# Optimization experiments

Measured on AMD Instinct MI355X. Metric: run time of the kernel, lower is better.

Reference implementation:

```python
import jax, jax.numpy as jnp
import numpy as np

B, T, P = 32, 40, 12
E, H = 2048, 1024
A_DIM, ACT_DIM = 9, 8


def _xavier(key, shape):
    fan_out, fan_in = shape
    lim = float(np.sqrt(6.0 / (fan_in + fan_out)))
    return jax.random.uniform(key, shape, jnp.float32, -lim, lim)


def setup_inputs() -> dict:
    key = jax.random.key(0)
    ks = jax.random.split(key, 8)
    return {
        "feature": jax.random.normal(ks[0], (B, T, P, E), jnp.float32),
        "W_embed": _xavier(ks[1], (H, E)),
        "b_embed": jnp.zeros((H,), jnp.float32),
        "W_ih": _xavier(ks[2], (3 * H, H)),
        "W_hh": _xavier(ks[3], (3 * H, H)),
        "b_ih": jnp.zeros((3 * H,), jnp.float32),
        "b_hh": jnp.zeros((3 * H,), jnp.float32),
        "W_act": _xavier(ks[4], (A_DIM, H)),
        "b_act": jnp.zeros((A_DIM,), jnp.float32),
        "W_activ": _xavier(ks[5], (ACT_DIM, H)),
        "b_activ": jnp.zeros((ACT_DIM,), jnp.float32),
    }


def reference(feature, W_embed, b_embed, W_ih, W_hh, b_ih, b_hh,
              W_act, b_act, W_activ, b_activ):
    # embed: Linear + Tanh -> [B, T, P, H]
    x = jnp.tanh(jnp.einsum('btpe,he->btph', feature, W_embed) + b_embed)
    # precompute input-side GRU gates for all timesteps: [B, T, P, 3H]
    gx = jnp.einsum('btph,gh->btpg', x, W_ih) + b_ih

    def step(h, gx_t):  # h: [B, P, H], gx_t: [B, P, 3H]
        gh = jnp.einsum('bph,gh->bpg', h, W_hh) + b_hh
        xr, xz, xn = jnp.split(gx_t, 3, axis=-1)
        hr, hz, hn = jnp.split(gh, 3, axis=-1)
        r = jax.nn.sigmoid(xr + hr)
        z = jax.nn.sigmoid(xz + hz)
        n = jnp.tanh(xn + r * hn)
        h_new = (1.0 - z) * n + z * h
        return h_new, h_new

    h0 = jnp.zeros((feature.shape[0], feature.shape[2], W_hh.shape[1]), feature.dtype)
    _, hs = jax.lax.scan(step, h0, jnp.moveaxis(gx, 1, 0))  # hs: [T, B, P, H]
    hiddens = jnp.moveaxis(hs, 0, 1)  # [B, T, P, H]

    # per-person action logits; torch loop order is (batch, time, person)
    action_logits = (jnp.einsum('btph,ah->btpa', hiddens, W_act) + b_act
                     ).reshape(-1, W_act.shape[0])
    # MaxPool2d((P,1)) over person axis, then Linear
    pooled = hiddens.max(axis=2)  # [B, T, H]
    activity_logits = (jnp.einsum('bth,ah->bta', pooled, W_activ) + b_activ
                       ).reshape(-1, W_activ.shape[0])
    return action_logits, activity_logits
```

## Files before the change

### kernel.cpp

```cpp
#include <hip/hip_runtime.h>
#include <cstdint>

#define B_ 32
#define T_ 40
#define P_ 12
#define E_ 2048
#define H_ 1024
#define BP 384
#define M_ 15360

typedef _Float16 f16;
typedef _Float16 f16x8 __attribute__((ext_vector_type(8)));
typedef float f32x4 __attribute__((ext_vector_type(4)));

__device__ __forceinline__ void cp16(const void* g, void* l) {
    auto gp = (const __attribute__((address_space(1))) uint32_t*)(uintptr_t)g;
    auto lp = (__attribute__((address_space(3))) uint32_t*)(uint32_t)(uintptr_t)l;
    __builtin_amdgcn_global_load_lds(gp, lp, 16, 0, 0);
}

__device__ __forceinline__ void store_wt(f16* p, f16 v) {
    unsigned short u = __builtin_bit_cast(unsigned short, v);
    asm volatile("global_store_short %0, %1, off sc0 sc1" :: "v"(p), "v"(u) : "memory");
}

__device__ __forceinline__ float fast_tanh(float x) {
    return 1.f - 2.f / (__expf(2.f * x) + 1.f);
}
__device__ __forceinline__ float fast_sig(float x) {
    return 1.f / (1.f + __expf(-x));
}

#define CVT_N0 ((M_ * E_) / 8)
#define CVT_N1 (CVT_N0 + (H_ * E_) / 8)
#define CVT_N2 (CVT_N1 + (3 * H_ * H_) / 8)
#define CVT_N3 (CVT_N2 + (3 * H_ * H_) / 8)
__global__ __launch_bounds__(256) void cvt_all(const float* __restrict__ f,
                                               const float* __restrict__ we,
                                               const float* __restrict__ wih,
                                               const float* __restrict__ whh,
                                               f16* __restrict__ fo, f16* __restrict__ weo,
                                               f16* __restrict__ wiho, f16* __restrict__ whho) {
    int i = blockIdx.x * 256 + threadIdx.x;
    if (i >= CVT_N3) return;
    const float* src; f16* dst; int j;
    if (i < CVT_N0)      { src = f;   dst = fo;   j = i; }
    else if (i < CVT_N1) { src = we;  dst = weo;  j = i - CVT_N0; }
    else if (i < CVT_N2) { src = wih; dst = wiho; j = i - CVT_N1; }
    else                 { src = whh; dst = whho; j = i - CVT_N2; }
    const float4* in4 = (const float4*)src;
    float4 a = in4[2 * j], b = in4[2 * j + 1];
    f16x8 o = {(f16)a.x, (f16)a.y, (f16)a.z, (f16)a.w,
               (f16)b.x, (f16)b.y, (f16)b.z, (f16)b.w};
    ((f16x8*)dst)[j] = o;
}

template <int EPI>
__global__ __launch_bounds__(256) void gemm128(const f16* __restrict__ A,
                                               const f16* __restrict__ Bm,
                                               const float* __restrict__ bias,
                                               f16* __restrict__ out, int K, int N) {
    __shared__ f16 As[2][128 * 32];
    __shared__ f16 Bs[2][128 * 32];
    const int tid = threadIdx.x;
    const int w = tid >> 6, l = tid & 63;
    const int wm = w >> 1, wn = w & 1;
    const long arow0 = (long)blockIdx.x * 128;
    const long brow0 = (long)blockIdx.y * 128;
    const int srow = l >> 2, scol = (l & 3) * 8;

    const f16* aptr = A + (arow0 + srow) * (long)K + scol;
    const f16* bptr = Bm + (brow0 + srow) * (long)K + scol;

    f32x4 acc[4][4] = {};

#pragma unroll
    for (int s = 0; s < 2; ++s) {
        int slice = w + s * 4;
        cp16(aptr + (long)slice * 16 * K, (void*)(As[0] + slice * 512));
        cp16(bptr + (long)slice * 16 * K, (void*)(Bs[0] + slice * 512));
    }
    asm volatile("s_waitcnt vmcnt(0)" ::: "memory");
    __syncthreads();

    const int nt = K >> 5;
    for (int t = 0; t < nt; ++t) {
        const int cur = t & 1;
        if (t + 1 < nt) {
            const long k0 = (long)(t + 1) << 5;
#pragma unroll
            for (int s = 0; s < 2; ++s) {
                int slice = w + s * 4;
                cp16(aptr + (long)slice * 16 * K + k0, (void*)(As[cur ^ 1] + slice * 512));
                cp16(bptr + (long)slice * 16 * K + k0, (void*)(Bs[cur ^ 1] + slice * 512));
            }
        }
        f16x8 af[4], bf[4];
#pragma unroll
        for (int i = 0; i < 4; ++i)
            af[i] = *(const f16x8*)(As[cur] + (wm * 64 + i * 16 + (l & 15)) * 32 + (l >> 4) * 8);
#pragma unroll
        for (int j = 0; j < 4; ++j)
            bf[j] = *(const f16x8*)(Bs[cur] + (wn * 64 + j * 16 + (l & 15)) * 32 + (l >> 4) * 8);
#pragma unroll
        for (int i = 0; i < 4; ++i)
#pragma unroll
            for (int j = 0; j < 4; ++j)
                acc[i][j] = __builtin_amdgcn_mfma_f32_16x16x32_f16(af[i], bf[j], acc[i][j], 0, 0, 0);
        asm volatile("s_waitcnt vmcnt(0)" ::: "memory");
        __syncthreads();
    }

    const int colq = l & 15, rowq = (l >> 4) * 4;
#pragma unroll
    for (int i = 0; i < 4; ++i)
#pragma unroll
        for (int j = 0; j < 4; ++j)
#pragma unroll
            for (int r = 0; r < 4; ++r) {
                long m = arow0 + wm * 64 + i * 16 + rowq + r;
                int n = (int)brow0 + wn * 64 + j * 16 + colq;
                float v = acc[i][j][r] + bias[n];
                if (EPI == 0) {
                    out[m * N + n] = (f16)fast_tanh(v);
                } else {
                    int b = (int)(m / (T_ * P_));
                    int rem = (int)(m % (T_ * P_));
                    int t = rem / P_, p = rem % P_;
                    out[((long)t * BP + b * P_ + p) * N + n] = (f16)v;
                }
            }
}

__global__ __launch_bounds__(256) void gru_step(const f16* __restrict__ h16_in,
                                                f16* __restrict__ h16_out,
                                                float* __restrict__ h32,
                                                const f16* __restrict__ Whh,
                                                const float* __restrict__ b_hh,
                                                const f16* __restrict__ gx16,
                                                f16* __restrict__ hid16, int t) {
    __shared__ f16 As[32 * 32];
    __shared__ f16 Bs[3 * 64 * 32];
    const int tid = threadIdx.x;
    const int w = tid >> 6, l = tid & 63;
    const int m0 = blockIdx.x * 32, n0 = blockIdx.y * 64;
    const int srow = l >> 2, scol = (l & 3) * 8;

    f32x4 acc[3][2] = {};

    for (int k0 = 0; k0 < H_; k0 += 32) {
        __syncthreads();
        if (w < 2)
            cp16(h16_in + (m0 + w * 16 + srow) * H_ + k0 + scol, (void*)(As + w * 512));
#pragma unroll
        for (int q3 = 0; q3 < 3; ++q3) {
            int s = w + q3 * 4;
            int g = s >> 2, q = s & 3;
            cp16(Whh + (long)(g * H_ + n0 + q * 16 + srow) * H_ + k0 + scol,
                 (void*)(Bs + (g * 64 + q * 16) * 32));
        }
        __syncthreads();
        f16x8 af[2], bf[3];
#pragma unroll
        for (int i = 0; i < 2; ++i)
            af[i] = *(const f16x8*)(As + (i * 16 + (l & 15)) * 32 + (l >> 4) * 8);
#pragma unroll
        for (int g = 0; g < 3; ++g)
            bf[g] = *(const f16x8*)(Bs + (g * 64 + w * 16 + (l & 15)) * 32 + (l >> 4) * 8);
#pragma unroll
        for (int g = 0; g < 3; ++g)
#pragma unroll
            for (int i = 0; i < 2; ++i)
                acc[g][i] = __builtin_amdgcn_mfma_f32_16x16x32_f16(af[i], bf[g], acc[g][i], 0, 0, 0);
    }

    const int col = n0 + w * 16 + (l & 15);
    const long gxbase = (long)t * BP * 3072;
    const float bhr = b_hh[col], bhz = b_hh[H_ + col], bhn = b_hh[2 * H_ + col];
#pragma unroll
    for (int i = 0; i < 2; ++i)
#pragma unroll
        for (int r = 0; r < 4; ++r) {
            int m = m0 + i * 16 + (l >> 4) * 4 + r;
            float hr = acc[0][i][r] + bhr;
            float hz = acc[1][i][r] + bhz;
            float hn = acc[2][i][r] + bhn;
            long gxrow = gxbase + (long)m * 3072;
            float xr = (float)gx16[gxrow + col];
            float xz = (float)gx16[gxrow + H_ + col];
            float xn = (float)gx16[gxrow + 2 * H_ + col];
            float rr = fast_sig(xr + hr);
            float zz = fast_sig(xz + hz);
            float nn = fast_tanh(xn + rr * hn);
            float hp = h32[m * H_ + col];
            float hnew = (1.f - zz) * nn + zz * hp;
            h32[m * H_ + col] = hnew;
            h16_out[m * H_ + col] = (f16)hnew;
            int b = m / P_, p = m % P_;
            hid16[(((long)b * T_ + t) * P_ + p) * H_ + col] = (f16)hnew;
        }
}

#define GRU_GRID 256
#define GRU_THREADS 384
#define GRU_BLDS (48 * 1024 * 2)
#define GRU_ALDS (4 * 96 * 64 * 2)
#define GRU_LDS (GRU_BLDS + GRU_ALDS)
#define FLAG_STRIDE 16

__global__ __launch_bounds__(GRU_THREADS) void gru_persistent(
        const f16* __restrict__ Whh, const float* __restrict__ bhh,
        const f16* __restrict__ gx16, f16* __restrict__ hid16,
        int* __restrict__ flags) {
    extern __shared__ char lds[];
    char* const Asb = lds + GRU_BLDS;

    const int tid = threadIdx.x;
    const int w = tid >> 6, l = tid & 63;
    const int q = l >> 4;

    const int bid = blockIdx.x;
    const int x = bid & 7;
    const int rg = x >> 1;
    const int nb = (x & 1) * 32 + (bid >> 3);
    const int m0 = rg * 96;
    const int j0 = nb * 16;

    for (int c = tid; c < 6144; c += GRU_THREADS) {
        int r = c >> 7;
        int kc = (c & 127) * 8;
        int grow = (r >> 4) * H_ + j0 + (r & 15);
        f16x8 v = *(const f16x8*)(Whh + (long)grow * H_ + kc);
        *(f16x8*)(lds + r * 2048 + ((kc * 2) ^ ((r & 7) << 4))) = v;
    }

    const int arow_l = w * 16 + (l & 15);
    int a_off[2], b_off[3][2];
#pragma unroll
    for (int sub = 0; sub < 2; ++sub) {
        a_off[sub] = arow_l * 128 + (((sub * 32 + q * 8) * 2) ^ ((arow_l & 7) << 4));
#pragma unroll
        for (int g = 0; g < 3; ++g) {
            int br = g * 16 + (l & 15);
            b_off[g][sub] = br * 2048 + (((sub * 32 + q * 8) * 2) ^ ((br & 7) << 4));
        }
    }
    const int swz = ((l & 7) ^ (l >> 3)) << 3;
    const int mA1 = m0 + w * 16 + (l >> 3);
    const int mA2 = mA1 + 8;
    const long srcA1 = ((long)(mA1 / P_) * T_ * P_ + (mA1 % P_)) * H_ + swz;
    const long srcA2 = ((long)(mA2 / P_) * T_ * P_ + (mA2 % P_)) * H_ + swz;

    const int col = j0 + (l & 15);
    const float bhr = bhh[col], bhz = bhh[H_ + col], bhn = bhh[2 * H_ + col];
    const int mrow = m0 + w * 16 + q * 4;
    long dstrow[4];
#pragma unroll
    for (int r = 0; r < 4; ++r) {
        int m = mrow + r;
        dstrow[r] = ((long)(m / P_) * T_ * P_ + (m % P_)) * H_ + col;
    }

    float hval[4] = {0.f, 0.f, 0.f, 0.f};

    f16 pgr[4], pgz[4], pgn[4];
#pragma unroll
    for (int r = 0; r < 4; ++r) {
        const long row = (long)(mrow + r) * 3072 + col;
        pgr[r] = gx16[row];
        pgz[r] = gx16[row + H_];
        pgn[r] = gx16[row + 2 * H_];
    }
    __syncthreads();

    for (int t = 0; t < T_; ++t) {
        f32x4 acc0 = {}, acc1 = {}, acc2 = {};

        if (t > 0) {
            if (w == 0) {
                const int* fp = flags + (((rg << 6) + l) * FLAG_STRIDE);
                while (__hip_atomic_load(fp, __ATOMIC_RELAXED,
                                         __HIP_MEMORY_SCOPE_AGENT) < t) {
                    __builtin_amdgcn_s_sleep(2);
                }
                __builtin_amdgcn_fence(__ATOMIC_ACQUIRE, "agent");
            }
            __syncthreads();

            const f16* __restrict__ hsrc = hid16 + (long)(t - 1) * (P_ * H_);

#pragma unroll
            for (int s = 0; s < 3; ++s) {
                char* b = Asb + s * 12288 + w * 2048;
                cp16(hsrc + srcA1 + s * 64, b);
                cp16(hsrc + srcA2 + s * 64, b + 1024);
            }

#pragma unroll
            for (int kk = 0; kk < 16; ++kk) {
                asm volatile("s_waitcnt lgkmcnt(0)" ::: "memory");
                if (kk < 13) {
                    const int s = kk + 3;
                    char* b = Asb + (s & 3) * 12288 + w * 2048;
                    cp16(hsrc + srcA1 + s * 64, b);
                    cp16(hsrc + srcA2 + s * 64, b + 1024);
                    asm volatile("s_waitcnt vmcnt(6)" ::: "memory");
                } else if (kk == 13) {
                    asm volatile("s_waitcnt vmcnt(4)" ::: "memory");
                } else if (kk == 14) {
                    asm volatile("s_waitcnt vmcnt(2)" ::: "memory");
                } else {
                    asm volatile("s_waitcnt vmcnt(0)" ::: "memory");
                }
                __builtin_amdgcn_sched_barrier(0);
                const char* Ab = Asb + (kk & 3) * 12288;
#pragma unroll
                for (int sub = 0; sub < 2; ++sub) {
                    f16x8 af  = *(const f16x8*)(Ab + a_off[sub]);
                    f16x8 bf0 = *(const f16x8*)(lds + b_off[0][sub] + kk * 128);
                    f16x8 bf1 = *(const f16x8*)(lds + b_off[1][sub] + kk * 128);
                    f16x8 bf2 = *(const f16x8*)(lds + b_off[2][sub] + kk * 128);
                    acc0 = __builtin_amdgcn_mfma_f32_16x16x32_f16(af, bf0, acc0, 0, 0, 0);
                    acc1 = __builtin_amdgcn_mfma_f32_16x16x32_f16(af, bf1, acc1, 0, 0, 0);
                    acc2 = __builtin_amdgcn_mfma_f32_16x16x32_f16(af, bf2, acc2, 0, 0, 0);
                }
            }
        }

        const long toff = (long)t * (P_ * H_);
#pragma unroll
        for (int r = 0; r < 4; ++r) {
            float hr = acc0[r] + bhr;
            float hz = acc1[r] + bhz;
            float hn = acc2[r] + bhn;
            float rr = fast_sig((float)pgr[r] + hr);
            float zz = fast_sig((float)pgz[r] + hz);
            float nn = fast_tanh((float)pgn[r] + rr * hn);
            float hnew = (1.f - zz) * nn + zz * hval[r];
            hval[r] = hnew;
            store_wt(hid16 + toff + dstrow[r], (f16)hnew);
        }
        asm volatile("s_waitcnt vmcnt(0)" ::: "memory");
        __syncthreads();
        if (tid == 0) {
            __hip_atomic_store(flags + (((rg << 6) + nb) * FLAG_STRIDE), t + 1,
                               __ATOMIC_RELEASE, __HIP_MEMORY_SCOPE_AGENT);
        }

        if (t + 1 < T_) {
            const long gxb = (long)(t + 1) * BP * 3072 + col;
#pragma unroll
            for (int r = 0; r < 4; ++r) {
                const long row = gxb + (long)(mrow + r) * 3072;
                pgr[r] = gx16[row];
                pgz[r] = gx16[row + H_];
                pgn[r] = gx16[row + 2 * H_];
            }
        }
    }
}

__global__ __launch_bounds__(256) void logits_kernel(const f16* __restrict__ hid16,
                                                     const float* __restrict__ W_act,
                                                     const float* __restrict__ b_act,
                                                     const float* __restrict__ W_activ,
                                                     const float* __restrict__ b_activ,
                                                     float* __restrict__ out) {
    __shared__ f16 hs[P_ * H_];
    __shared__ float pooled[H_];
    const int bt = blockIdx.x;
    const int tid = threadIdx.x, w = tid >> 6, l = tid & 63;

    const f16x8* src = (const f16x8*)(hid16 + (long)bt * P_ * H_);
    f16x8* dst = (f16x8*)hs;
    for (int i = tid; i < P_ * H_ / 8; i += 256) dst[i] = src[i];
    __syncthreads();

    for (int i = tid; i < H_; i += 256) {
        float mx = (float)hs[i];
#pragma unroll
        for (int p = 1; p < P_; ++p) mx = fmaxf(mx, (float)hs[p * H_ + i]);
        pooled[i] = mx;
    }
    __syncthreads();

    for (int j = w; j < 108; j += 4) {
        int p = j / 9, a = j % 9;
        float s = 0.f;
#pragma unroll
        for (int it = 0; it < 16; ++it) {
            int idx = l + it * 64;
            s += (float)hs[p * H_ + idx] * W_act[a * H_ + idx];
        }
#pragma unroll
        for (int off = 32; off > 0; off >>= 1) s += __shfl_down(s, off);
        if (l == 0) out[((long)bt * P_ + p) * 9 + a] = s + b_act[a];
    }
    for (int j = w; j < 8; j += 4) {
        float s = 0.f;
#pragma unroll
        for (int it = 0; it < 16; ++it) {
            int idx = l + it * 64;
            s += pooled[idx] * W_activ[j * H_ + idx];
        }
#pragma unroll
        for (int off = 32; off > 0; off >>= 1) s += __shfl_down(s, off);
        if (l == 0) out[(long)M_ * 9 + (long)bt * 8 + j] = s + b_activ[j];
    }
}

extern "C" void kernel_launch(void* const* d_in, const int* in_sizes, int n_in,
                              void* d_out, int out_size, void* d_ws, size_t ws_size,
                              hipStream_t stream) {
    const float* feature = (const float*)d_in[0];
    const float* W_embed = (const float*)d_in[1];
    const float* b_embed = (const float*)d_in[2];
    const float* W_ih    = (const float*)d_in[3];
    const float* W_hh    = (const float*)d_in[4];
    const float* b_ih    = (const float*)d_in[5];
    const float* b_hh    = (const float*)d_in[6];
    const float* W_act   = (const float*)d_in[7];
    const float* b_act   = (const float*)d_in[8];
    const float* W_activ = (const float*)d_in[9];
    const float* b_activ = (const float*)d_in[10];
    float* out = (float*)d_out;

    char* ws = (char*)d_ws;
    size_t off = 0;
    auto alloc = [&](size_t bytes) {
        void* p = ws + off;
        off = (off + bytes + 255) & ~(size_t)255;
        return p;
    };
    f16*   feat16 = (f16*)alloc((size_t)M_ * E_ * 2);
    f16*   wE16   = (f16*)alloc((size_t)H_ * E_ * 2);
    f16*   wIH16  = (f16*)alloc((size_t)3 * H_ * H_ * 2);
    f16*   wHH16  = (f16*)alloc((size_t)3 * H_ * H_ * 2);
    f16*   x16    = (f16*)alloc((size_t)M_ * H_ * 2);
    f16*   gx16   = (f16*)alloc((size_t)M_ * 3 * H_ * 2);
    float* h32    = (float*)alloc((size_t)BP * H_ * 4);
    f16*   h16a   = (f16*)alloc((size_t)BP * H_ * 2);
    f16*   h16b   = (f16*)alloc((size_t)BP * H_ * 2);
    f16*   hid16  = (f16*)alloc((size_t)M_ * H_ * 2);
    int*   flags  = (int*)h32;
    (void)ws_size; (void)in_sizes; (void)n_in; (void)out_size;

    cvt_all<<<CVT_N3 / 256, 256, 0, stream>>>(feature, W_embed, W_ih, W_hh,
                                              feat16, wE16, wIH16, wHH16);

    gemm128<0><<<dim3(M_ / 128, H_ / 128), 256, 0, stream>>>(feat16, wE16, b_embed, x16, E_, H_);
    gemm128<1><<<dim3(M_ / 128, (3 * H_) / 128), 256, 0, stream>>>(x16, wIH16, b_ih, gx16, H_, 3 * H_);

    hipMemsetAsync(h32, 0, (size_t)BP * H_ * 4 + (size_t)BP * H_ * 2, stream);

    (void)hipFuncSetAttribute(reinterpret_cast<const void*>(gru_persistent),
                              hipFuncAttributeMaxDynamicSharedMemorySize, GRU_LDS);
    const f16* p_whh = wHH16; const float* p_bhh = b_hh; const f16* p_gx = gx16;
    f16* p_hid = hid16; int* p_flags = flags;
    void* kargs[] = {&p_whh, &p_bhh, &p_gx, &p_hid, &p_flags};
    hipError_t cerr = hipLaunchCooperativeKernel(
        reinterpret_cast<const void*>(gru_persistent),
        dim3(GRU_GRID), dim3(GRU_THREADS), kargs, GRU_LDS, stream);
    if (cerr != hipSuccess) {
        for (int t = 0; t < T_; ++t) {
            const f16* hin = (t & 1) ? h16b : h16a;
            f16* hout = (t & 1) ? h16a : h16b;
            gru_step<<<dim3(BP / 32, H_ / 64), 256, 0, stream>>>(hin, hout, h32, wHH16, b_hh,
                                                                 gx16, hid16, t);
        }
    }

    logits_kernel<<<B_ * T_, 256, 0, stream>>>(hid16, W_act, b_act, W_activ, b_activ, out);
}
```

Before: 929.5 us.

## Load GRU hidden-state operand straight into registers and relax store ordering

The recurrent GEMM in the persistent GRU kernel now loads the previous hidden state directly from global memory into registers: all 32 16-byte chunks are issued up front and then fed to the MFMAs. This replaces the 4-stage LDS ring filled with global_load_lds and its manual vmcnt/lgkmcnt waits. The hidden-state stores become plain stores instead of write-through sc0/sc1 stores, and the explicit vmcnt(0) wait before the flag release is dropped. The next step's gate prefetch now happens before the barrier and flag publication. The aim is to cut per-step latency on the serial recurrence, at the cost of higher register pressure. Publishing the flag without draining the stores may weaken cross-block visibility of the new hidden state.

```diff
diff --git a/kernel.cpp b/kernel.cpp
--- a/kernel.cpp
+++ b/kernel.cpp
@@ -17,11 +17,6 @@
     auto gp = (const __attribute__((address_space(1))) uint32_t*)(uintptr_t)g;
     auto lp = (__attribute__((address_space(3))) uint32_t*)(uint32_t)(uintptr_t)l;
     __builtin_amdgcn_global_load_lds(gp, lp, 16, 0, 0);
-}
-
-__device__ __forceinline__ void store_wt(f16* p, f16 v) {
-    unsigned short u = __builtin_bit_cast(unsigned short, v);
-    asm volatile("global_store_short %0, %1, off sc0 sc1" :: "v"(p), "v"(u) : "memory");
 }
 
 __device__ __forceinline__ float fast_tanh(float x) {
@@ -203,9 +198,7 @@
 
 #define GRU_GRID 256
 #define GRU_THREADS 384
-#define GRU_BLDS (48 * 1024 * 2)
-#define GRU_ALDS (4 * 96 * 64 * 2)
-#define GRU_LDS (GRU_BLDS + GRU_ALDS)
+#define GRU_LDS (48 * 1024 * 2)
 #define FLAG_STRIDE 16
 
 __global__ __launch_bounds__(GRU_THREADS) void gru_persistent(
@@ -213,7 +206,6 @@
         const f16* __restrict__ gx16, f16* __restrict__ hid16,
         int* __restrict__ flags) {
     extern __shared__ char lds[];
-    char* const Asb = lds + GRU_BLDS;
 
     const int tid = threadIdx.x;
     const int w = tid >> 6, l = tid & 63;
@@ -234,22 +226,17 @@
         *(f16x8*)(lds + r * 2048 + ((kc * 2) ^ ((r & 7) << 4))) = v;
     }
 
-    const int arow_l = w * 16 + (l & 15);
-    int a_off[2], b_off[3][2];
-#pragma unroll
-    for (int sub = 0; sub < 2; ++sub) {
-        a_off[sub] = arow_l * 128 + (((sub * 32 + q * 8) * 2) ^ ((arow_l & 7) << 4));
+    int b_off[3][2];
+#pragma unroll
+    for (int sub = 0; sub < 2; ++sub)
 #pragma unroll
         for (int g = 0; g < 3; ++g) {
             int br = g * 16 + (l & 15);
             b_off[g][sub] = br * 2048 + (((sub * 32 + q * 8) * 2) ^ ((br & 7) << 4));
         }
-    }
-    const int swz = ((l & 7) ^ (l >> 3)) << 3;
-    const int mA1 = m0 + w * 16 + (l >> 3);
-    const int mA2 = mA1 + 8;
-    const long srcA1 = ((long)(mA1 / P_) * T_ * P_ + (mA1 % P_)) * H_ + swz;
-    const long srcA2 = ((long)(mA2 / P_) * T_ * P_ + (mA2 % P_)) * H_ + swz;
+
+    const int mA = m0 + w * 16 + (l & 15);
+    const long arow_base = ((long)(mA / P_) * (T_ * P_) + (mA % P_)) * H_ + q * 8;
 
     const int col = j0 + (l & 15);
     const float bhr = bhh[col], bhz = bhh[H_ + col], bhn = bhh[2 * H_ + col];
@@ -287,42 +274,24 @@
             }
             __syncthreads();
 
-            const f16* __restrict__ hsrc = hid16 + (long)(t - 1) * (P_ * H_);
-
-#pragma unroll
-            for (int s = 0; s < 3; ++s) {
-                char* b = Asb + s * 12288 + w * 2048;
-                cp16(hsrc + srcA1 + s * 64, b);
-                cp16(hsrc + srcA2 + s * 64, b + 1024);
-            }
-
+            const f16* __restrict__ ap = hid16 + (long)(t - 1) * (P_ * H_) + arow_base;
+            f16x8 areg[16][2];
 #pragma unroll
             for (int kk = 0; kk < 16; ++kk) {
-                asm volatile("s_waitcnt lgkmcnt(0)" ::: "memory");
-                if (kk < 13) {
-                    const int s = kk + 3;
-                    char* b = Asb + (s & 3) * 12288 + w * 2048;
-                    cp16(hsrc + srcA1 + s * 64, b);
-                    cp16(hsrc + srcA2 + s * 64, b + 1024);
-                    asm volatile("s_waitcnt vmcnt(6)" ::: "memory");
-                } else if (kk == 13) {
-                    asm volatile("s_waitcnt vmcnt(4)" ::: "memory");
-                } else if (kk == 14) {
-                    asm volatile("s_waitcnt vmcnt(2)" ::: "memory");
-                } else {
-                    asm volatile("s_waitcnt vmcnt(0)" ::: "memory");
-                }
-                __builtin_amdgcn_sched_barrier(0);
-                const char* Ab = Asb + (kk & 3) * 12288;
+                areg[kk][0] = *(const f16x8*)(ap + kk * 64);
+                areg[kk][1] = *(const f16x8*)(ap + kk * 64 + 32);
+            }
+
+#pragma unroll
+            for (int kk = 0; kk < 16; ++kk) {
 #pragma unroll
                 for (int sub = 0; sub < 2; ++sub) {
-                    f16x8 af  = *(const f16x8*)(Ab + a_off[sub]);
                     f16x8 bf0 = *(const f16x8*)(lds + b_off[0][sub] + kk * 128);
                     f16x8 bf1 = *(const f16x8*)(lds + b_off[1][sub] + kk * 128);
                     f16x8 bf2 = *(const f16x8*)(lds + b_off[2][sub] + kk * 128);
-                    acc0 = __builtin_amdgcn_mfma_f32_16x16x32_f16(af, bf0, acc0, 0, 0, 0);
-                    acc1 = __builtin_amdgcn_mfma_f32_16x16x32_f16(af, bf1, acc1, 0, 0, 0);
-                    acc2 = __builtin_amdgcn_mfma_f32_16x16x32_f16(af, bf2, acc2, 0, 0, 0);
+                    acc0 = __builtin_amdgcn_mfma_f32_16x16x32_f16(areg[kk][sub], bf0, acc0, 0, 0, 0);
+                    acc1 = __builtin_amdgcn_mfma_f32_16x16x32_f16(areg[kk][sub], bf1, acc1, 0, 0, 0);
+                    acc2 = __builtin_amdgcn_mfma_f32_16x16x32_f16(areg[kk][sub], bf2, acc2, 0, 0, 0);
                 }
             }
         }
@@ -338,13 +307,7 @@
             float nn = fast_tanh((float)pgn[r] + rr * hn);
             float hnew = (1.f - zz) * nn + zz * hval[r];
             hval[r] = hnew;
-            store_wt(hid16 + toff + dstrow[r], (f16)hnew);
-        }
-        asm volatile("s_waitcnt vmcnt(0)" ::: "memory");
-        __syncthreads();
-        if (tid == 0) {
-            __hip_atomic_store(flags + (((rg << 6) + nb) * FLAG_STRIDE), t + 1,
-                               __ATOMIC_RELEASE, __HIP_MEMORY_SCOPE_AGENT);
+            hid16[toff + dstrow[r]] = (f16)hnew;
         }
 
         if (t + 1 < T_) {
@@ -356,6 +319,12 @@
                 pgz[r] = gx16[row + H_];
                 pgn[r] = gx16[row + 2 * H_];
             }
+        }
+
+        __syncthreads();
+        if (tid == 0) {
+            __hip_atomic_store(flags + (((rg << 6) + nb) * FLAG_STRIDE), t + 1,
+                               __ATOMIC_RELEASE, __HIP_MEMORY_SCOPE_AGENT);
         }
     }
 }
```

Measured after the change: 1.018 ms. 9.5% more time.
